# Optimization experiments

Measured on AMD Instinct MI355X. Metric: run time of the kernel, lower is better.

The kernel has to match this reference:

```python
import jax, jax.numpy as jnp
import numpy as np

# Irrep layout of node_vec: 128x0e | 64x1e (64*3) | 32x2e (32*5)
MUL0, MUL1, MUL2 = 128, 64, 32
A = 32  # node_attr scalar channels (32x0e)
N = 8192


def setup_inputs() -> dict:
    key = jax.random.key(0)
    ks = jax.random.split(key, 12)
    f32 = jnp.float32
    return {
        "node_vec": jax.random.normal(ks[0], (N, MUL0 + 3 * MUL1 + 5 * MUL2), f32),
        "node_embedding": jax.random.normal(ks[1], (N, A), f32),
        # fctp_1: TP(input, attr) -> gated irreps (scalars + gates + vectors)
        "W1s": jax.random.normal(ks[2], (MUL0, A, MUL0), f32),          # 0e x 0e -> 0e
        "b1s": jnp.zeros((MUL0,), f32),
        "W1g": jax.random.normal(ks[3], (MUL0, A, MUL1 + MUL2), f32),   # 0e x 0e -> gate 0e
        "b1g": jnp.zeros((MUL1 + MUL2,), f32),
        "W1v1": jax.random.normal(ks[4], (MUL1, A, MUL1), f32),         # 1e x 0e -> 1e
        "W1v2": jax.random.normal(ks[5], (MUL2, A, MUL2), f32),         # 2e x 0e -> 2e
        # fctp_2: TP(mlp_mid, attr) -> 32x0e (only scalar path allowed by CG rules)
        "W2": jax.random.normal(ks[6], (MUL0, A, A), f32),
        "b2": jnp.zeros((A,), f32),
        # output network: LinearRS(32->32) + SiLU + LinearRS(32->1)
        "W3": jax.random.normal(ks[7], (A, A), f32),
        "b3": jnp.zeros((A,), f32),
        "W4": jax.random.normal(ks[8], (A, 1), f32),
        "b4": jnp.zeros((1,), f32),
    }


def reference(node_vec, node_embedding, W1s, b1s, W1g, b1g, W1v1, W1v2, W2, b2, W3, b3, W4, b4):
    n = node_vec.shape[0]
    attr = node_embedding
    # split features by irrep degree
    s = node_vec[:, :MUL0]                                         # [n,128]   0e
    v1 = node_vec[:, MUL0:MUL0 + 3 * MUL1].reshape(n, MUL1, 3)     # [n,64,3]  1e
    v2 = node_vec[:, MUL0 + 3 * MUL1:].reshape(n, MUL2, 5)         # [n,32,5]  2e

    inv = lambda u: 1.0 / np.sqrt(u * A).astype(np.float32)

    # ---- fctp_1: fully-connected TP with scalar attr (l x 0e -> l per-path mixing) ----
    s_mid = jnp.einsum('nu,nv,uvw->nw', s, attr, W1s) * inv(MUL0) + b1s
    g = jnp.einsum('nu,nv,uvw->nw', s, attr, W1g) * inv(MUL0) + b1g
    v1_mid = jnp.einsum('num,nv,uvw->nwm', v1, attr, W1v1) * inv(MUL1)
    v2_mid = jnp.einsum('num,nv,uvw->nwm', v2, attr, W1v2) * inv(MUL2)

    # ---- SwishGate: SiLU on scalars, sigmoid gates on vectors ----
    s_act = jax.nn.silu(s_mid)
    gate = jax.nn.sigmoid(g)
    v1_g = v1_mid * gate[:, :MUL1, None]
    v2_g = v2_mid * gate[:, MUL1:, None]
    # NOTE: v1_g/v2_g have no allowed CG path into the 0e output of fctp_2 (l x 0 -> 0
    # only for l=0), so they do not contribute — exactly as in the original module.
    del v1_g, v2_g

    # ---- fctp_2: mlp_mid x attr -> 32x0e (scalar path only) ----
    h = jnp.einsum('nu,nv,uvw->nw', s_act, attr, W2) * inv(MUL0) + b2

    # ---- output network: LinearRS + SiLU + LinearRS ----
    h = jax.nn.silu(h @ (W3 / np.sqrt(A).astype(np.float32)) + b3)
    pred_energy = h @ (W4 / np.sqrt(A).astype(np.float32)) + b4     # [n,1]
    return pred_energy
```

## Files before the change

### kernel.cpp

```cpp
#include <hip/hip_runtime.h>

typedef _Float16 f16;
typedef f16 f16x8 __attribute__((ext_vector_type(8)));
typedef f16 f16x4 __attribute__((ext_vector_type(4)));
typedef f16 f16x2 __attribute__((ext_vector_type(2)));
typedef float f32x4 __attribute__((ext_vector_type(4)));

union F8 { uint4 u4; f16x8 v; f16x2 h[4]; f16 e[8]; };

__global__ __launch_bounds__(256) void prep_kernel(
    const float* __restrict__ W1s, const float* __restrict__ W2,
    f16* __restrict__ W1P, f16* __restrict__ W2P)
{
    __shared__ f16 T[32 * 36];
    const int b = blockIdx.x, t = threadIdx.x;

    const float* src; f16* dst; int u, w0, W;
    if (b < 512) { u = b >> 2; w0 = (b & 3) * 32; W = 128; src = W1s; dst = W1P; }
    else         { u = b - 512; w0 = 0;           W = 32;  src = W2;  dst = W2P; }
    {
        int v = t >> 3, wq = t & 7;
        float4 f = *(const float4*)(src + (size_t)(u * 32 + v) * W + w0 + wq * 4);
        T[v * 36 + wq * 4 + 0] = (f16)f.x;
        T[v * 36 + wq * 4 + 1] = (f16)f.y;
        T[v * 36 + wq * 4 + 2] = (f16)f.z;
        T[v * 36 + wq * 4 + 3] = (f16)f.w;
    }
    __syncthreads();
    {
        int w = t >> 3, vr = t & 7;
        f16x4 o = { T[(vr * 4 + 0) * 36 + w], T[(vr * 4 + 1) * 36 + w],
                    T[(vr * 4 + 2) * 36 + w], T[(vr * 4 + 3) * 36 + w] };
        *(f16x4*)(dst + (size_t)u * (W * 32) + (size_t)(w0 + w) * 32 + vr * 4) = o;
    }
}

__global__ __launch_bounds__(256, 2) void gemm1_kernel(
    const float* __restrict__ node_vec, const float* __restrict__ attr,
    const f16* __restrict__ W1P, const float* __restrict__ b1s,
    f16* __restrict__ s_act)
{
    __shared__ alignas(16) f16 s_lds[32 * 136];

    const int t  = threadIdx.x;
    const int n0 = blockIdx.x * 32;
    const int l  = t & 63, lr = l & 15, q = l >> 4;
    const int c0 = blockIdx.y * 64 + (t >> 6) * 16;

    #pragma unroll
    for (int i = 0; i < 4; ++i) {
        int idx = t + 256 * i;
        int r = idx >> 5, c4 = idx & 31;
        float4 f = *(const float4*)(node_vec + (size_t)(n0 + r) * 480 + c4 * 4);
        f16x4 o = { (f16)f.x, (f16)f.y, (f16)f.z, (f16)f.w };
        *(f16x4*)(s_lds + r * 136 + c4 * 4) = o;
    }

    F8 af0, af1;
    #pragma unroll
    for (int kk = 0; kk < 4; ++kk) {
        float2 fa = *(const float2*)(attr + (size_t)(n0 + lr) * 32 + q * 8 + kk * 2);
        float2 fb = *(const float2*)(attr + (size_t)(n0 + 16 + lr) * 32 + q * 8 + kk * 2);
        af0.h[kk] = f16x2{ (f16)fa.x, (f16)fa.y };
        af1.h[kk] = f16x2{ (f16)fb.x, (f16)fb.y };
    }

    const f16* Bp = W1P + ((size_t)(c0 + lr)) * 32 + q * 8;
    f16x8 B[8];
    #pragma unroll
    for (int j = 0; j < 8; ++j)
        B[j] = *(const f16x8*)(Bp + (size_t)j * 4096);

    __syncthreads();

    f32x4 acc0 = {0.f, 0.f, 0.f, 0.f}, acc1 = {0.f, 0.f, 0.f, 0.f};

    F8 s8[2][2];
    s8[0][0].v = *(const f16x8*)(s_lds + lr * 136);
    s8[0][1].v = *(const f16x8*)(s_lds + (16 + lr) * 136);

    #pragma unroll
    for (int uo = 0; uo < 16; ++uo) {
        const int cur = uo & 1, nxt = cur ^ 1;
        const int uon = (uo + 1 < 16) ? uo + 1 : 15;
        s8[nxt][0].v = *(const f16x8*)(s_lds + lr * 136 + uon * 8);
        s8[nxt][1].v = *(const f16x8*)(s_lds + (16 + lr) * 136 + uon * 8);
        #pragma unroll
        for (int j = 0; j < 8; ++j) {
            const int u = uo * 8 + j;
            f16x8 bf = B[j];
            const int un = (u + 8 < 128) ? (u + 8) : u;
            B[j] = *(const f16x8*)(Bp + (size_t)un * 4096);
            f16 sv0 = s8[cur][0].e[j];
            f16 sv1 = s8[cur][1].e[j];
            f16x2 sb0 = { sv0, sv0 }, sb1 = { sv1, sv1 };
            F8 a0, a1;
            #pragma unroll
            for (int kk = 0; kk < 4; ++kk) {
                a0.h[kk] = sb0 * af0.h[kk];
                a1.h[kk] = sb1 * af1.h[kk];
            }
            acc0 = __builtin_amdgcn_mfma_f32_16x16x32_f16(a0.v, bf, acc0, 0, 0, 0);
            acc1 = __builtin_amdgcn_mfma_f32_16x16x32_f16(a1.v, bf, acc1, 0, 0, 0);
        }
    }

    const float bv = b1s[c0 + lr];
    #pragma unroll
    for (int reg = 0; reg < 4; ++reg) {
        float v0 = acc0[reg] * 0.015625f + bv;
        float v1 = acc1[reg] * 0.015625f + bv;
        s_act[(size_t)(n0 + q * 4 + reg) * 128 + c0 + lr] =
            (f16)(v0 / (1.f + __expf(-v0)));
        s_act[(size_t)(n0 + 16 + q * 4 + reg) * 128 + c0 + lr] =
            (f16)(v1 / (1.f + __expf(-v1)));
    }
}

__global__ __launch_bounds__(256, 2) void gemm2_head_kernel(
    const f16* __restrict__ s_act, const float* __restrict__ attr,
    const f16* __restrict__ W2P, const float* __restrict__ b2,
    const float* __restrict__ W3, const float* __restrict__ b3,
    const float* __restrict__ W4, const float* __restrict__ b4,
    float* __restrict__ out)
{
    __shared__ alignas(16) f16 s_lds[32 * 136];
    __shared__ alignas(16) float red[4][32 * 36];
    __shared__ alignas(16) float W3_lds[32 * 36];
    __shared__ alignas(16) float h_lds[32 * 36];

    const int t  = threadIdx.x;
    const int n0 = blockIdx.x * 32;
    const int wv = t >> 6, l = t & 63, lr = l & 15, q = l >> 4;
    const int u0 = wv * 32;

    const f16* B2p = W2P + ((size_t)u0 * 32 + lr) * 32 + q * 8;
    f16x8 B0[8], B1[8];
    #pragma unroll
    for (int j = 0; j < 8; ++j) {
        B0[j] = *(const f16x8*)(B2p + (size_t)j * 1024);
        B1[j] = *(const f16x8*)(B2p + (size_t)j * 1024 + 512);
    }

    F8 af0, af1;
    #pragma unroll
    for (int kk = 0; kk < 4; ++kk) {
        float2 fa = *(const float2*)(attr + (size_t)(n0 + lr) * 32 + q * 8 + kk * 2);
        float2 fb = *(const float2*)(attr + (size_t)(n0 + 16 + lr) * 32 + q * 8 + kk * 2);
        af0.h[kk] = f16x2{ (f16)fa.x, (f16)fa.y };
        af1.h[kk] = f16x2{ (f16)fb.x, (f16)fb.y };
    }

    #pragma unroll
    for (int i = 0; i < 2; ++i) {
        int ch = t + 256 * i;
        int r = ch >> 4, c8 = ch & 15;
        *(uint4*)(s_lds + r * 136 + c8 * 8) =
            *(const uint4*)(s_act + (size_t)(n0 + r) * 128 + c8 * 8);
    }
    { int i = t >> 3, jj = (t & 7) * 4;
      *(f32x4*)(W3_lds + i * 36 + jj) = *(const f32x4*)(W3 + i * 32 + jj); }
    __syncthreads();

    f32x4 acc00 = {0,0,0,0}, acc01 = {0,0,0,0};
    f32x4 acc10 = {0,0,0,0}, acc11 = {0,0,0,0};

    F8 s8[2][2];
    s8[0][0].v = *(const f16x8*)(s_lds + lr * 136 + u0);
    s8[0][1].v = *(const f16x8*)(s_lds + (16 + lr) * 136 + u0);

    #pragma unroll
    for (int uo = 0; uo < 4; ++uo) {
        const int cur = uo & 1, nxt = cur ^ 1;
        const int uon = (uo + 1 < 4) ? uo + 1 : 3;
        s8[nxt][0].v = *(const f16x8*)(s_lds + lr * 136 + u0 + uon * 8);
        s8[nxt][1].v = *(const f16x8*)(s_lds + (16 + lr) * 136 + u0 + uon * 8);
        #pragma unroll
        for (int j = 0; j < 8; ++j) {
            const int k = uo * 8 + j;
            f16x8 bf0 = B0[j], bf1 = B1[j];
            const int kn = (k + 8 < 32) ? (k + 8) : k;
            B0[j] = *(const f16x8*)(B2p + (size_t)kn * 1024);
            B1[j] = *(const f16x8*)(B2p + (size_t)kn * 1024 + 512);
            f16 sv0 = s8[cur][0].e[j];
            f16 sv1 = s8[cur][1].e[j];
            f16x2 sb0 = { sv0, sv0 }, sb1 = { sv1, sv1 };
            F8 a0, a1;
            #pragma unroll
            for (int kk = 0; kk < 4; ++kk) {
                a0.h[kk] = sb0 * af0.h[kk];
                a1.h[kk] = sb1 * af1.h[kk];
            }
            acc00 = __builtin_amdgcn_mfma_f32_16x16x32_f16(a0.v, bf0, acc00, 0, 0, 0);
            acc01 = __builtin_amdgcn_mfma_f32_16x16x32_f16(a0.v, bf1, acc01, 0, 0, 0);
            acc10 = __builtin_amdgcn_mfma_f32_16x16x32_f16(a1.v, bf0, acc10, 0, 0, 0);
            acc11 = __builtin_amdgcn_mfma_f32_16x16x32_f16(a1.v, bf1, acc11, 0, 0, 0);
        }
    }

    #pragma unroll
    for (int reg = 0; reg < 4; ++reg) {
        red[wv][(q * 4 + reg) * 36 + lr]           = acc00[reg];
        red[wv][(q * 4 + reg) * 36 + 16 + lr]      = acc01[reg];
        red[wv][(16 + q * 4 + reg) * 36 + lr]      = acc10[reg];
        red[wv][(16 + q * 4 + reg) * 36 + 16 + lr] = acc11[reg];
    }
    __syncthreads();

    {
        int row = t >> 3, c4 = (t & 7) * 4;
        f32x4 s = *(const f32x4*)(&red[0][row * 36 + c4]);
        s = s + *(const f32x4*)(&red[1][row * 36 + c4]);
        s = s + *(const f32x4*)(&red[2][row * 36 + c4]);
        s = s + *(const f32x4*)(&red[3][row * 36 + c4]);
        #pragma unroll
        for (int e = 0; e < 4; ++e)
            h_lds[row * 36 + c4 + e] = s[e] * 0.015625f + b2[c4 + e];
    }
    __syncthreads();

    {
        int node = t >> 3, j4 = (t & 7) * 4;
        float a0 = 0.f, a1 = 0.f, a2 = 0.f, a3 = 0.f;
        #pragma unroll
        for (int i = 0; i < 32; ++i) {
            float hv = h_lds[node * 36 + i];
            a0 += hv * W3_lds[i * 36 + j4 + 0];
            a1 += hv * W3_lds[i * 36 + j4 + 1];
            a2 += hv * W3_lds[i * 36 + j4 + 2];
            a3 += hv * W3_lds[i * 36 + j4 + 3];
        }
        const float inv = 0.17677669529663687f;
        float p = 0.f;
        float aa[4] = { a0, a1, a2, a3 };
        #pragma unroll
        for (int e = 0; e < 4; ++e) {
            float tv = aa[e] * inv + b3[j4 + e];
            float g  = tv / (1.f + __expf(-tv));
            p += g * W4[j4 + e] * inv;
        }
        p += __shfl_xor(p, 1);
        p += __shfl_xor(p, 2);
        p += __shfl_xor(p, 4);
        if ((t & 7) == 0) out[n0 + node] = p + b4[0];
    }
}

extern "C" void kernel_launch(void* const* d_in, const int* in_sizes, int n_in,
                              void* d_out, int out_size, void* d_ws, size_t ws_size,
                              hipStream_t stream)
{
    const float* node_vec = (const float*)d_in[0];
    const float* attr     = (const float*)d_in[1];
    const float* W1s      = (const float*)d_in[2];
    const float* b1s      = (const float*)d_in[3];
    const float* W2       = (const float*)d_in[8];
    const float* b2       = (const float*)d_in[9];
    const float* W3       = (const float*)d_in[10];
    const float* b3       = (const float*)d_in[11];
    const float* W4       = (const float*)d_in[12];
    const float* b4       = (const float*)d_in[13];
    float* out = (float*)d_out;

    char* ws = (char*)d_ws;
    f16* W1P   = (f16*)(ws);
    f16* W2P   = (f16*)(ws + (1u << 20));
    f16* s_act = (f16*)(ws + (1280u << 10));

    prep_kernel<<<640, 256, 0, stream>>>(W1s, W2, W1P, W2P);
    gemm1_kernel<<<dim3(256, 2), 256, 0, stream>>>(node_vec, attr, W1P, b1s, s_act);
    gemm2_head_kernel<<<256, 256, 0, stream>>>(s_act, attr, W2P, b2,
                                               W3, b3, W4, b4, out);
}
```

Measured before the change: 114.6 us.

## Fuse both tensor-product GEMMs and output head into one kernel

Merges the first TP GEMM and the second TP GEMM plus head into a single 512-thread kernel, with each block handling 32 nodes and all 128 output channels across 8 waves. The SiLU activations stay in LDS rather than going through a global f16 buffer, which removes one launch and a global round-trip. Node_vec is now loaded once per node tile instead of twice. The second GEMM's reduction is split across 8 waves of 16 channels each, with an 8-way LDS reduction. In exchange, the grid shrinks from 512+256 blocks to 256 blocks with higher LDS use per block, which may lower occupancy and latency hiding.

```diff
diff --git a/kernel.cpp b/kernel.cpp
--- a/kernel.cpp
+++ b/kernel.cpp
@@ -35,25 +35,37 @@
     }
 }
 
-__global__ __launch_bounds__(256, 2) void gemm1_kernel(
+__global__ __launch_bounds__(512, 2) void fused_kernel(
     const float* __restrict__ node_vec, const float* __restrict__ attr,
     const f16* __restrict__ W1P, const float* __restrict__ b1s,
-    f16* __restrict__ s_act)
+    const f16* __restrict__ W2P, const float* __restrict__ b2,
+    const float* __restrict__ W3, const float* __restrict__ b3,
+    const float* __restrict__ W4, const float* __restrict__ b4,
+    float* __restrict__ out)
 {
-    __shared__ alignas(16) f16 s_lds[32 * 136];
+    __shared__ alignas(16) f16   s_lds[32 * 136];
+    __shared__ alignas(16) f16   sact_lds[32 * 136];
+    __shared__ alignas(16) float red[8][32 * 36];
+    __shared__ alignas(16) float W3_lds[32 * 36];
+    __shared__ alignas(16) float h_lds[32 * 36];
 
     const int t  = threadIdx.x;
     const int n0 = blockIdx.x * 32;
-    const int l  = t & 63, lr = l & 15, q = l >> 4;
-    const int c0 = blockIdx.y * 64 + (t >> 6) * 16;
-
-    #pragma unroll
-    for (int i = 0; i < 4; ++i) {
-        int idx = t + 256 * i;
+    const int wv = t >> 6, l = t & 63, lr = l & 15, q = l >> 4;
+    const int c0 = wv * 16;
+    const int u0 = wv * 16;
+
+    #pragma unroll
+    for (int i = 0; i < 2; ++i) {
+        int idx = t + 512 * i;
         int r = idx >> 5, c4 = idx & 31;
         float4 f = *(const float4*)(node_vec + (size_t)(n0 + r) * 480 + c4 * 4);
         f16x4 o = { (f16)f.x, (f16)f.y, (f16)f.z, (f16)f.w };
         *(f16x4*)(s_lds + r * 136 + c4 * 4) = o;
+    }
+    if (t < 256) {
+        int i = t >> 3, jj = (t & 7) * 4;
+        *(f32x4*)(W3_lds + i * 36 + jj) = *(const f32x4*)(W3 + i * 32 + jj);
     }
 
     F8 af0, af1;
@@ -89,8 +101,8 @@
         for (int j = 0; j < 8; ++j) {
             const int u = uo * 8 + j;
             f16x8 bf = B[j];
-            const int un = (u + 8 < 128) ? (u + 8) : u;
-            B[j] = *(const f16x8*)(Bp + (size_t)un * 4096);
+            if (u + 8 < 128)
+                B[j] = *(const f16x8*)(Bp + (size_t)(u + 8) * 4096);
             f16 sv0 = s8[cur][0].e[j];
             f16 sv1 = s8[cur][1].e[j];
             f16x2 sb0 = { sv0, sv0 }, sb1 = { sv1, sv1 };
@@ -105,34 +117,16 @@
         }
     }
 
-    const float bv = b1s[c0 + lr];
-    #pragma unroll
-    for (int reg = 0; reg < 4; ++reg) {
-        float v0 = acc0[reg] * 0.015625f + bv;
-        float v1 = acc1[reg] * 0.015625f + bv;
-        s_act[(size_t)(n0 + q * 4 + reg) * 128 + c0 + lr] =
-            (f16)(v0 / (1.f + __expf(-v0)));
-        s_act[(size_t)(n0 + 16 + q * 4 + reg) * 128 + c0 + lr] =
-            (f16)(v1 / (1.f + __expf(-v1)));
-    }
-}
-
-__global__ __launch_bounds__(256, 2) void gemm2_head_kernel(
-    const f16* __restrict__ s_act, const float* __restrict__ attr,
-    const f16* __restrict__ W2P, const float* __restrict__ b2,
-    const float* __restrict__ W3, const float* __restrict__ b3,
-    const float* __restrict__ W4, const float* __restrict__ b4,
-    float* __restrict__ out)
-{
-    __shared__ alignas(16) f16 s_lds[32 * 136];
-    __shared__ alignas(16) float red[4][32 * 36];
-    __shared__ alignas(16) float W3_lds[32 * 36];
-    __shared__ alignas(16) float h_lds[32 * 36];
-
-    const int t  = threadIdx.x;
-    const int n0 = blockIdx.x * 32;
-    const int wv = t >> 6, l = t & 63, lr = l & 15, q = l >> 4;
-    const int u0 = wv * 32;
+    {
+        const float bv = b1s[c0 + lr];
+        #pragma unroll
+        for (int reg = 0; reg < 4; ++reg) {
+            float v0 = acc0[reg] * 0.015625f + bv;
+            float v1 = acc1[reg] * 0.015625f + bv;
+            sact_lds[(q * 4 + reg) * 136 + c0 + lr]        = (f16)(v0 / (1.f + __expf(-v0)));
+            sact_lds[(16 + q * 4 + reg) * 136 + c0 + lr]   = (f16)(v1 / (1.f + __expf(-v1)));
+        }
+    }
 
     const f16* B2p = W2P + ((size_t)u0 * 32 + lr) * 32 + q * 8;
     f16x8 B0[8], B1[8];
@@ -142,48 +136,31 @@
         B1[j] = *(const f16x8*)(B2p + (size_t)j * 1024 + 512);
     }
 
-    F8 af0, af1;
-    #pragma unroll
-    for (int kk = 0; kk < 4; ++kk) {
-        float2 fa = *(const float2*)(attr + (size_t)(n0 + lr) * 32 + q * 8 + kk * 2);
-        float2 fb = *(const float2*)(attr + (size_t)(n0 + 16 + lr) * 32 + q * 8 + kk * 2);
-        af0.h[kk] = f16x2{ (f16)fa.x, (f16)fa.y };
-        af1.h[kk] = f16x2{ (f16)fb.x, (f16)fb.y };
-    }
-
-    #pragma unroll
-    for (int i = 0; i < 2; ++i) {
-        int ch = t + 256 * i;
-        int r = ch >> 4, c8 = ch & 15;
-        *(uint4*)(s_lds + r * 136 + c8 * 8) =
-            *(const uint4*)(s_act + (size_t)(n0 + r) * 128 + c8 * 8);
-    }
-    { int i = t >> 3, jj = (t & 7) * 4;
-      *(f32x4*)(W3_lds + i * 36 + jj) = *(const f32x4*)(W3 + i * 32 + jj); }
     __syncthreads();
 
     f32x4 acc00 = {0,0,0,0}, acc01 = {0,0,0,0};
     f32x4 acc10 = {0,0,0,0}, acc11 = {0,0,0,0};
 
-    F8 s8[2][2];
-    s8[0][0].v = *(const f16x8*)(s_lds + lr * 136 + u0);
-    s8[0][1].v = *(const f16x8*)(s_lds + (16 + lr) * 136 + u0);
-
-    #pragma unroll
-    for (int uo = 0; uo < 4; ++uo) {
+    F8 t8[2][2];
+    t8[0][0].v = *(const f16x8*)(sact_lds + lr * 136 + u0);
+    t8[0][1].v = *(const f16x8*)(sact_lds + (16 + lr) * 136 + u0);
+
+    #pragma unroll
+    for (int uo = 0; uo < 2; ++uo) {
         const int cur = uo & 1, nxt = cur ^ 1;
-        const int uon = (uo + 1 < 4) ? uo + 1 : 3;
-        s8[nxt][0].v = *(const f16x8*)(s_lds + lr * 136 + u0 + uon * 8);
-        s8[nxt][1].v = *(const f16x8*)(s_lds + (16 + lr) * 136 + u0 + uon * 8);
+        const int uon = (uo + 1 < 2) ? uo + 1 : 1;
+        t8[nxt][0].v = *(const f16x8*)(sact_lds + lr * 136 + u0 + uon * 8);
+        t8[nxt][1].v = *(const f16x8*)(sact_lds + (16 + lr) * 136 + u0 + uon * 8);
         #pragma unroll
         for (int j = 0; j < 8; ++j) {
             const int k = uo * 8 + j;
             f16x8 bf0 = B0[j], bf1 = B1[j];
-            const int kn = (k + 8 < 32) ? (k + 8) : k;
-            B0[j] = *(const f16x8*)(B2p + (size_t)kn * 1024);
-            B1[j] = *(const f16x8*)(B2p + (size_t)kn * 1024 + 512);
-            f16 sv0 = s8[cur][0].e[j];
-            f16 sv1 = s8[cur][1].e[j];
+            if (k + 8 < 16) {
+                B0[j] = *(const f16x8*)(B2p + (size_t)(k + 8) * 1024);
+                B1[j] = *(const f16x8*)(B2p + (size_t)(k + 8) * 1024 + 512);
+            }
+            f16 sv0 = t8[cur][0].e[j];
+            f16 sv1 = t8[cur][1].e[j];
             f16x2 sb0 = { sv0, sv0 }, sb1 = { sv1, sv1 };
             F8 a0, a1;
             #pragma unroll
@@ -208,41 +185,41 @@
     __syncthreads();
 
     {
-        int row = t >> 3, c4 = (t & 7) * 4;
-        f32x4 s = *(const f32x4*)(&red[0][row * 36 + c4]);
-        s = s + *(const f32x4*)(&red[1][row * 36 + c4]);
-        s = s + *(const f32x4*)(&red[2][row * 36 + c4]);
-        s = s + *(const f32x4*)(&red[3][row * 36 + c4]);
-        #pragma unroll
-        for (int e = 0; e < 4; ++e)
-            h_lds[row * 36 + c4 + e] = s[e] * 0.015625f + b2[c4 + e];
-    }
-    __syncthreads();
-
-    {
-        int node = t >> 3, j4 = (t & 7) * 4;
-        float a0 = 0.f, a1 = 0.f, a2 = 0.f, a3 = 0.f;
+        int row = t >> 4, c2 = (t & 15) * 2;
+        float s0 = 0.f, s1 = 0.f;
+        #pragma unroll
+        for (int w = 0; w < 8; ++w) {
+            s0 += red[w][row * 36 + c2];
+            s1 += red[w][row * 36 + c2 + 1];
+        }
+        h_lds[row * 36 + c2]     = s0 * 0.015625f + b2[c2];
+        h_lds[row * 36 + c2 + 1] = s1 * 0.015625f + b2[c2 + 1];
+    }
+    __syncthreads();
+
+    {
+        int node = t >> 4, jj = (t & 15) * 2;
+        float a0 = 0.f, a1 = 0.f;
         #pragma unroll
         for (int i = 0; i < 32; ++i) {
             float hv = h_lds[node * 36 + i];
-            a0 += hv * W3_lds[i * 36 + j4 + 0];
-            a1 += hv * W3_lds[i * 36 + j4 + 1];
-            a2 += hv * W3_lds[i * 36 + j4 + 2];
-            a3 += hv * W3_lds[i * 36 + j4 + 3];
+            a0 += hv * W3_lds[i * 36 + jj];
+            a1 += hv * W3_lds[i * 36 + jj + 1];
         }
         const float inv = 0.17677669529663687f;
         float p = 0.f;
-        float aa[4] = { a0, a1, a2, a3 };
-        #pragma unroll
-        for (int e = 0; e < 4; ++e) {
-            float tv = aa[e] * inv + b3[j4 + e];
+        float aa[2] = { a0, a1 };
+        #pragma unroll
+        for (int e = 0; e < 2; ++e) {
+            float tv = aa[e] * inv + b3[jj + e];
             float g  = tv / (1.f + __expf(-tv));
-            p += g * W4[j4 + e] * inv;
+            p += g * W4[jj + e] * inv;
         }
         p += __shfl_xor(p, 1);
         p += __shfl_xor(p, 2);
         p += __shfl_xor(p, 4);
-        if ((t & 7) == 0) out[n0 + node] = p + b4[0];
+        p += __shfl_xor(p, 8);
+        if ((t & 15) == 0) out[n0 + node] = p + b4[0];
     }
 }
 
@@ -263,12 +240,10 @@
     float* out = (float*)d_out;
 
     char* ws = (char*)d_ws;
-    f16* W1P   = (f16*)(ws);
-    f16* W2P   = (f16*)(ws + (1u << 20));
-    f16* s_act = (f16*)(ws + (1280u << 10));
+    f16* W1P = (f16*)(ws);
+    f16* W2P = (f16*)(ws + (1u << 20));
 
     prep_kernel<<<640, 256, 0, stream>>>(W1s, W2, W1P, W2P);
-    gemm1_kernel<<<dim3(256, 2), 256, 0, stream>>>(node_vec, attr, W1P, b1s, s_act);
-    gemm2_head_kernel<<<256, 256, 0, stream>>>(s_act, attr, W2P, b2,
-                                               W3, b3, W4, b4, out);
+    fused_kernel<<<256, 512, 0, stream>>>(node_vec, attr, W1P, b1s,
+                                          W2P, b2, W3, b3, W4, b4, out);
 }
```

New measurement: 109.7 us. 1.04x faster.
